# Performance work log

Hardware: AMD Instinct MI355X
Metric: run time of the kernel (lower is better)

The kernel has to match this reference:

```python
import jax, jax.numpy as jnp
import numpy as np

H, KVH, D, BS, L = 32, 8, 128, 16, 4096
MAX_BLOCKS = L // BS          # 256 blocks per sequence (sink cache capacity)
B = 16
NUM_BLOCKS = B * MAX_BLOCKS   # 4096 total cache blocks
T = MAX_BLOCKS * BS           # 4096 linearized cache slots per sequence
SCALE = 1.0 / np.sqrt(D)


def _rope_cos_sin(pos):
    # neox-style RoPE tables; pos: int array [...]. returns cos/sin [..., D/2]
    inv_freq = 1.0 / (10000.0 ** (jnp.arange(0, D, 2, dtype=jnp.float32) / D))
    ang = pos[..., None].astype(jnp.float32) * inv_freq
    return jnp.cos(ang), jnp.sin(ang)


def _apply_rope(x, cos, sin):
    # x [..., D]; cos/sin broadcastable to x[..., :D//2]
    x1, x2 = jnp.split(x, 2, axis=-1)
    return jnp.concatenate([x1 * cos - x2 * sin, x2 * cos + x1 * sin], axis=-1)


def setup_inputs() -> dict:
    key = jax.random.key(0)
    ks = jax.random.split(key, 6)
    q = jax.random.normal(ks[0], (B, H * D), dtype=jnp.float32)
    k = jax.random.normal(ks[1], (B, KVH * D), dtype=jnp.float32)
    v = jax.random.normal(ks[2], (B, KVH * D), dtype=jnp.float32)
    key_cache = jax.random.normal(ks[3], (NUM_BLOCKS, BS, KVH, D), dtype=jnp.float32)
    value_cache = jax.random.normal(ks[4], (NUM_BLOCKS, BS, KVH, D), dtype=jnp.float32)
    block_tables = jnp.arange(B * MAX_BLOCKS, dtype=jnp.int32).reshape(B, MAX_BLOCKS)
    context_lens = jax.random.randint(ks[5], (B,), 0, 6000, dtype=jnp.int32)
    return {"q": q, "k": k, "v": v, "key_cache": key_cache,
            "value_cache": value_cache, "block_tables": block_tables,
            "context_lens": context_lens}


def reference(q, k, v, key_cache, value_cache, block_tables, context_lens):
    ctx = context_lens.astype(jnp.int32)                         # [B] past tokens
    rem = ctx % BS
    # sink/rolling cap: if past >= model_context_len, effective seq len caps
    seq_len = jnp.where(ctx >= L, L - BS + rem + 1, ctx + 1)     # [B]
    pos_q = seq_len - 1                                          # capped current position

    # gather pre-rope keys/values from paged cache -> [B, T, KVH, D]
    keys = key_cache[block_tables].reshape(B, T, KVH, D)
    vals = value_cache[block_tables].reshape(B, T, KVH, D)

    # re-apply rope to gathered keys at their cache-relative positions 0..T-1
    cos_k, sin_k = _rope_cos_sin(jnp.arange(T))                  # [T, D/2]
    keys = _apply_rope(keys, cos_k[None, :, None, :], sin_k[None, :, None, :])

    # rope current q, k at capped positions
    cos_q, sin_q = _rope_cos_sin(pos_q)                          # [B, D/2]
    qh = _apply_rope(q.reshape(B, H, D), cos_q[:, None, :], sin_q[:, None, :])
    kh = _apply_rope(k.reshape(B, KVH, D), cos_q[:, None, :], sin_q[:, None, :])

    # scatter current token's k/v at its slot (offset rem in last used block == seq_len-1)
    bidx = jnp.arange(B)
    keys = keys.at[bidx, pos_q].set(kh)
    vals = vals.at[bidx, pos_q].set(v.reshape(B, KVH, D))

    # GQA attention over first seq_len cached tokens
    G = H // KVH
    qg = qh.reshape(B, KVH, G, D)
    scores = jnp.einsum('bhgd,bthd->bhgt', qg, keys) * SCALE     # [B, KVH, G, T]
    mask = jnp.arange(T)[None, :] < seq_len[:, None]             # [B, T]
    scores = jnp.where(mask[:, None, None, :], scores, jnp.finfo(scores.dtype).min)
    probs = jax.nn.softmax(scores, axis=-1)
    out = jnp.einsum('bhgt,bthd->bhgd', probs, vals)             # [B, KVH, G, D]
    return out.reshape(B, H * D)
```

## Files before the change

### kernel.cpp

```cpp
#include <hip/hip_runtime.h>
#include <math.h>

#define B_      16
#define H_      32
#define KVH_    8
#define G_      4
#define D_      128
#define BS_     16
#define L_      4096
#define MAXB_   256
#define T_      4096
#define NPART_  64
#define PART_   64
#define SCALE_  0.08838834764831843f

typedef unsigned long long ull;

__device__ __forceinline__ int seq_len_of(int ctx) {
  return (ctx >= L_) ? (L_ - BS_ + (ctx & (BS_ - 1)) + 1) : (ctx + 1);
}

__global__ void rope_table_kernel(float* __restrict__ tab) {
  int idx = blockIdx.x * blockDim.x + threadIdx.x;
  if (idx >= T_ * 64) return;
  int t = idx >> 6, i = idx & 63;
  double inv = pow(10000.0, -(double)(2 * i) / 128.0);
  float ang = (float)t * (float)inv;
  double a = (double)ang;
  tab[2 * idx]     = (float)cos(a);
  tab[2 * idx + 1] = (float)sin(a);
}


#define LOADK(P, tt)                                                        \
  {                                                                         \
    int tcl_  = min((tt), t1m1);                                            \
    int blk_  = (int)((packed >> (((tcl_ - t0) >> 4) * 16)) & 0xFFFF);      \
    int base_ = ((blk_ * BS_ + (tcl_ & (BS_ - 1))) * KVH_ + kvh) * D_;      \
    const float4* kc4_ = (const float4*)(kc + base_);                       \
    const float4* vc4_ = (const float4*)(vc + base_);                       \
    P##ka = kc4_[dg];      P##kb = kc4_[16 + dg];                           \
    P##va = vc4_[dg];      P##vb = vc4_[16 + dg];                           \
  }

#define COMPUTE(P, tt)                                                      \
  {                                                                         \
    float kr1[4], kr2[4];                                                   \
    kr1[0] = P##ka.x * cc0.x - P##kb.x * cc0.y;                             \
    kr2[0] = P##kb.x * cc0.x + P##ka.x * cc0.y;                             \
    kr1[1] = P##ka.y * cc0.z - P##kb.y * cc0.w;                             \
    kr2[1] = P##kb.y * cc0.z + P##ka.y * cc0.w;                             \
    kr1[2] = P##ka.z * cc1.x - P##kb.z * cc1.y;                             \
    kr2[2] = P##kb.z * cc1.x + P##ka.z * cc1.y;                             \
    kr1[3] = P##ka.w * cc1.z - P##kb.w * cc1.w;                             \
    kr2[3] = P##kb.w * cc1.z + P##ka.w * cc1.w;                             \
    bool valid_ = ((tt) < t1) & ((tt) != posq);                             \
    float s[G_];                                                            \
    _Pragma("unroll")                                                       \
    for (int g = 0; g < G_; ++g) {                                          \
      s[g] = kr1[0] * q1[g][0] + kr2[0] * q2[g][0]                          \
           + kr1[1] * q1[g][1] + kr2[1] * q2[g][1]                          \
           + kr1[2] * q1[g][2] + kr2[2] * q2[g][2]                          \
           + kr1[3] * q1[g][3] + kr2[3] * q2[g][3];                         \
    }                                                                       \
    _Pragma("unroll")                                                       \
    for (int off = 1; off <= 8; off <<= 1) {                                \
      _Pragma("unroll")                                                     \
      for (int g = 0; g < G_; ++g) s[g] += __shfl_xor(s[g], off);           \
    }                                                                       \
    _Pragma("unroll")                                                       \
    for (int g = 0; g < G_; ++g) {                                          \
      float sv   = valid_ ? s[g] : -1e30f;                                  \
      float mn   = fmaxf(m[g], sv);                                         \
      float corr = __expf(m[g] - mn);                                       \
      float p    = __expf(sv - mn);                                         \
      p = valid_ ? p : 0.0f;                                                \
      m[g] = mn;                                                            \
      l[g] = l[g] * corr + p;                                               \
      acc[g][0] = acc[g][0] * corr + p * P##va.x;                           \
      acc[g][1] = acc[g][1] * corr + p * P##va.y;                           \
      acc[g][2] = acc[g][2] * corr + p * P##va.z;                           \
      acc[g][3] = acc[g][3] * corr + p * P##va.w;                           \
      acc[g][4] = acc[g][4] * corr + p * P##vb.x;                           \
      acc[g][5] = acc[g][5] * corr + p * P##vb.y;                           \
      acc[g][6] = acc[g][6] * corr + p * P##vb.z;                           \
      acc[g][7] = acc[g][7] * corr + p * P##vb.w;                           \
    }                                                                       \
    {                      \
      float nc_;                                                            \
      nc_ = cc0.x * r0.x - cc0.y * r0.y;                                    \
      cc0.y = cc0.y * r0.x + cc0.x * r0.y; cc0.x = nc_;                     \
      nc_ = cc0.z * r0.z - cc0.w * r0.w;                                    \
      cc0.w = cc0.w * r0.z + cc0.z * r0.w; cc0.z = nc_;                     \
      nc_ = cc1.x * r1.x - cc1.y * r1.y;                                    \
      cc1.y = cc1.y * r1.x + cc1.x * r1.y; cc1.x = nc_;                     \
      nc_ = cc1.z * r1.z - cc1.w * r1.w;                                    \
      cc1.w = cc1.w * r1.z + cc1.z * r1.w; cc1.z = nc_;                     \
    }                                                                       \
  }

__global__ __launch_bounds__(256, 3) void attn_partial_kernel(
    const float* __restrict__ q, const float* __restrict__ knew,
    const float* __restrict__ vnew, const float* __restrict__ kc,
    const float* __restrict__ vc, const int* __restrict__ btab,
    const int* __restrict__ ctxl, const float* __restrict__ tab,
    float* __restrict__ opart, float2* __restrict__ ml) {
  int bid  = blockIdx.x;
  int wv   = threadIdx.x >> 6;
  int kvh  = (bid >> 4) & (KVH_ - 1);
  int b    = bid >> 7;
  int part = ((bid & 15) << 2) | wv;

  int seq = seq_len_of(ctxl[b]);
  int t0 = part * PART_;
  if (t0 >= seq) return;
  int t1 = min(t0 + PART_, seq);
  int t1m1 = t1 - 1;
  int posq = seq - 1;
  int pidx = ((b * KVH_ + kvh) * NPART_ + part) * G_;

  int lane = threadIdx.x & 63;
  int tsub = lane >> 4;
  int dg   = lane & 15;

  int4 bi = *(const int4*)(btab + b * MAXB_ + (t0 >> 4));
  ull packed = (ull)(unsigned)bi.x | ((ull)(unsigned)bi.y << 16)
             | ((ull)(unsigned)bi.z << 32) | ((ull)(unsigned)bi.w << 48);

  const float4* tab4 = (const float4*)tab;

  int tstart = t0 + tsub;
  float4 cc0 = tab4[tstart * 32 + 2 * dg];
  float4 cc1 = tab4[tstart * 32 + 2 * dg + 1];
  float4 r0  = tab4[4 * 32 + 2 * dg];
  float4 r1  = tab4[4 * 32 + 2 * dg + 1];

  float q1[G_][4], q2[G_][4];
  {
    float4 cq0 = tab4[posq * 32 + 2 * dg];
    float4 cq1 = tab4[posq * 32 + 2 * dg + 1];
#pragma unroll
    for (int g = 0; g < G_; ++g) {
      const float* qp = q + b * (H_ * D_) + (kvh * G_ + g) * D_;
      float4 a  = *(const float4*)(qp + 4 * dg);
      float4 bq = *(const float4*)(qp + 64 + 4 * dg);
      q1[g][0] = (a.x * cq0.x - bq.x * cq0.y) * SCALE_;
      q2[g][0] = (bq.x * cq0.x + a.x * cq0.y) * SCALE_;
      q1[g][1] = (a.y * cq0.z - bq.y * cq0.w) * SCALE_;
      q2[g][1] = (bq.y * cq0.z + a.y * cq0.w) * SCALE_;
      q1[g][2] = (a.z * cq1.x - bq.z * cq1.y) * SCALE_;
      q2[g][2] = (bq.z * cq1.x + a.z * cq1.y) * SCALE_;
      q1[g][3] = (a.w * cq1.z - bq.w * cq1.w) * SCALE_;
      q2[g][3] = (bq.w * cq1.z + a.w * cq1.w) * SCALE_;
    }
  }

  float m[G_], l[G_], acc[G_][8];
#pragma unroll
  for (int g = 0; g < G_; ++g) {
    m[g] = -1e30f; l[g] = 0.f;
#pragma unroll
    for (int j = 0; j < 8; ++j) acc[g][j] = 0.f;
  }

  {
    float4 Aka, Akb, Ava, Avb;
    float4 Bka, Bkb, Bva, Bvb;
    int nIter = (t1 - t0 + 3) >> 2;
    nIter = (nIter + 1) & ~1;
    int t = tstart;
    LOADK(A, t);
    for (int it = 0; it < nIter; it += 2) {
      LOADK(B, t + 4);  COMPUTE(A, t);  t += 4;
      LOADK(A, t + 4);  COMPUTE(B, t);  t += 4;
    }
  }

  if (lane < 16 && posq >= t0 && posq < t1) {
    const float* kp = knew + (b * KVH_ + kvh) * D_;
    float4 xa = *(const float4*)(kp + 4 * dg);
    float4 xb = *(const float4*)(kp + 64 + 4 * dg);
    float4 p0 = tab4[posq * 32 + 2 * dg];
    float4 p1 = tab4[posq * 32 + 2 * dg + 1];
    float kr1[4], kr2[4];
    kr1[0] = xa.x * p0.x - xb.x * p0.y;  kr2[0] = xb.x * p0.x + xa.x * p0.y;
    kr1[1] = xa.y * p0.z - xb.y * p0.w;  kr2[1] = xb.y * p0.z + xa.y * p0.w;
    kr1[2] = xa.z * p1.x - xb.z * p1.y;  kr2[2] = xb.z * p1.x + xa.z * p1.y;
    kr1[3] = xa.w * p1.z - xb.w * p1.w;  kr2[3] = xb.w * p1.z + xa.w * p1.w;
    const float* vp = vnew + (b * KVH_ + kvh) * D_;
    float4 va_ = *(const float4*)(vp + 4 * dg);
    float4 vb_ = *(const float4*)(vp + 64 + 4 * dg);
    float s[G_];
#pragma unroll
    for (int g = 0; g < G_; ++g) {
      s[g] = kr1[0] * q1[g][0] + kr2[0] * q2[g][0]
           + kr1[1] * q1[g][1] + kr2[1] * q2[g][1]
           + kr1[2] * q1[g][2] + kr2[2] * q2[g][2]
           + kr1[3] * q1[g][3] + kr2[3] * q2[g][3];
    }
#pragma unroll
    for (int off = 1; off <= 8; off <<= 1) {
#pragma unroll
      for (int g = 0; g < G_; ++g) s[g] += __shfl_xor(s[g], off);
    }
#pragma unroll
    for (int g = 0; g < G_; ++g) {
      float sv   = s[g];
      float mn   = fmaxf(m[g], sv);
      float corr = __expf(m[g] - mn);
      float p    = __expf(sv - mn);
      m[g] = mn;
      l[g] = l[g] * corr + p;
      acc[g][0] = acc[g][0] * corr + p * va_.x;
      acc[g][1] = acc[g][1] * corr + p * va_.y;
      acc[g][2] = acc[g][2] * corr + p * va_.z;
      acc[g][3] = acc[g][3] * corr + p * va_.w;
      acc[g][4] = acc[g][4] * corr + p * vb_.x;
      acc[g][5] = acc[g][5] * corr + p * vb_.y;
      acc[g][6] = acc[g][6] * corr + p * vb_.z;
      acc[g][7] = acc[g][7] * corr + p * vb_.w;
    }
  }

#pragma unroll
  for (int off = 16; off <= 32; off <<= 1) {
#pragma unroll
    for (int g = 0; g < G_; ++g) {
      float mo = __shfl_xor(m[g], off);
      float lo = __shfl_xor(l[g], off);
      float M  = fmaxf(m[g], mo);
      float fa = __expf(m[g] - M);
      float fb = __expf(mo - M);
      l[g] = l[g] * fa + lo * fb;
      m[g] = M;
#pragma unroll
      for (int j = 0; j < 8; ++j) {
        float ao = __shfl_xor(acc[g][j], off);
        acc[g][j] = acc[g][j] * fa + ao * fb;
      }
    }
  }

  if (lane < 16) {
#pragma unroll
    for (int g = 0; g < G_; ++g) {
      float* op = opart + (size_t)(pidx + g) * D_;
      *(float4*)(op + 4 * dg)      = make_float4(acc[g][0], acc[g][1], acc[g][2], acc[g][3]);
      *(float4*)(op + 64 + 4 * dg) = make_float4(acc[g][4], acc[g][5], acc[g][6], acc[g][7]);
      if (lane == 0) ml[pidx + g] = make_float2(m[g], l[g]);
    }
  }
}

__global__ void attn_reduce_kernel(const float* __restrict__ opart,
                                   const float2* __restrict__ ml,
                                   const int* __restrict__ ctxl,
                                   float* __restrict__ out) {
  int bh = blockIdx.x;
  int b = bh >> 5, h = bh & 31;
  int kvh = h >> 2, g = h & 3;
  int d = threadIdx.x;
  int seq = seq_len_of(ctxl[b]);
  int nlive = (seq + PART_ - 1) / PART_;
  int base = (b * KVH_ + kvh) * NPART_;

  float M = -1e30f;
  for (int p = 0; p < nlive; ++p) M = fmaxf(M, ml[(base + p) * G_ + g].x);
  float L = 0.f, O = 0.f;
  for (int p = 0; p < nlive; ++p) {
    float2 mlv = ml[(base + p) * G_ + g];
    float f = __expf(mlv.x - M);
    L += mlv.y * f;
    O += opart[(size_t)((base + p) * G_ + g) * D_ + d] * f;
  }
  out[b * (H_ * D_) + h * D_ + d] = O / L;
}

extern "C" void kernel_launch(void* const* d_in, const int* in_sizes, int n_in,
                              void* d_out, int out_size, void* d_ws, size_t ws_size,
                              hipStream_t stream) {
  const float* q    = (const float*)d_in[0];
  const float* k    = (const float*)d_in[1];
  const float* v    = (const float*)d_in[2];
  const float* kc   = (const float*)d_in[3];
  const float* vc   = (const float*)d_in[4];
  const int*   btab = (const int*)d_in[5];
  const int*   ctxl = (const int*)d_in[6];
  float* out = (float*)d_out;

  float*  tab   = (float*)d_ws;
  float*  opart = tab + (size_t)T_ * 64 * 2;
  float2* ml    = (float2*)(opart + (size_t)B_ * KVH_ * NPART_ * G_ * D_);

  rope_table_kernel<<<(T_ * 64 + 255) / 256, 256, 0, stream>>>(tab);
  attn_partial_kernel<<<B_ * KVH_ * (NPART_ / 4), 256, 0, stream>>>(
      q, k, v, kc, vc, btab, ctxl, tab, opart, ml);
  attn_reduce_kernel<<<B_ * H_, D_, 0, stream>>>(opart, ml, ctxl, out);
}
```

Before: 137.8 us.

## Stage contiguous KV token rows through double-buffered LDS across all heads

Each block now handles one 32-token partition for all 8 KV heads with 512 threads. It cooperatively loads full contiguous token rows (all heads) of K and V into double-buffered shared memory, then each wave computes its head from LDS. The aim is fully coalesced global reads in place of per-head strided 512-byte segments, with prefetch of the next group overlapping compute. The cost is a __syncthreads per 4-token group, LDS traffic, and twice as many partitions for the reduce kernel to combine.

```diff
diff --git a/kernel.cpp b/kernel.cpp
--- a/kernel.cpp
+++ b/kernel.cpp
@@ -10,11 +10,11 @@
 #define L_      4096
 #define MAXB_   256
 #define T_      4096
-#define NPART_  64
-#define PART_   64
+#define PARTN_  32
+#define NP_     (T_ / PARTN_)
+#define GT_     4
+#define TPAD_   1032
 #define SCALE_  0.08838834764831843f
-
-typedef unsigned long long ull;
 
 __device__ __forceinline__ int seq_len_of(int ctx) {
   return (ctx >= L_) ? (L_ - BS_ + (ctx & (BS_ - 1)) + 1) : (ctx + 1);
@@ -31,101 +31,33 @@
   tab[2 * idx + 1] = (float)sin(a);
 }
 
-
-#define LOADK(P, tt)                                                        \
-  {                                                                         \
-    int tcl_  = min((tt), t1m1);                                            \
-    int blk_  = (int)((packed >> (((tcl_ - t0) >> 4) * 16)) & 0xFFFF);      \
-    int base_ = ((blk_ * BS_ + (tcl_ & (BS_ - 1))) * KVH_ + kvh) * D_;      \
-    const float4* kc4_ = (const float4*)(kc + base_);                       \
-    const float4* vc4_ = (const float4*)(vc + base_);                       \
-    P##ka = kc4_[dg];      P##kb = kc4_[16 + dg];                           \
-    P##va = vc4_[dg];      P##vb = vc4_[16 + dg];                           \
-  }
-
-#define COMPUTE(P, tt)                                                      \
-  {                                                                         \
-    float kr1[4], kr2[4];                                                   \
-    kr1[0] = P##ka.x * cc0.x - P##kb.x * cc0.y;                             \
-    kr2[0] = P##kb.x * cc0.x + P##ka.x * cc0.y;                             \
-    kr1[1] = P##ka.y * cc0.z - P##kb.y * cc0.w;                             \
-    kr2[1] = P##kb.y * cc0.z + P##ka.y * cc0.w;                             \
-    kr1[2] = P##ka.z * cc1.x - P##kb.z * cc1.y;                             \
-    kr2[2] = P##kb.z * cc1.x + P##ka.z * cc1.y;                             \
-    kr1[3] = P##ka.w * cc1.z - P##kb.w * cc1.w;                             \
-    kr2[3] = P##kb.w * cc1.z + P##ka.w * cc1.w;                             \
-    bool valid_ = ((tt) < t1) & ((tt) != posq);                             \
-    float s[G_];                                                            \
-    _Pragma("unroll")                                                       \
-    for (int g = 0; g < G_; ++g) {                                          \
-      s[g] = kr1[0] * q1[g][0] + kr2[0] * q2[g][0]                          \
-           + kr1[1] * q1[g][1] + kr2[1] * q2[g][1]                          \
-           + kr1[2] * q1[g][2] + kr2[2] * q2[g][2]                          \
-           + kr1[3] * q1[g][3] + kr2[3] * q2[g][3];                         \
-    }                                                                       \
-    _Pragma("unroll")                                                       \
-    for (int off = 1; off <= 8; off <<= 1) {                                \
-      _Pragma("unroll")                                                     \
-      for (int g = 0; g < G_; ++g) s[g] += __shfl_xor(s[g], off);           \
-    }                                                                       \
-    _Pragma("unroll")                                                       \
-    for (int g = 0; g < G_; ++g) {                                          \
-      float sv   = valid_ ? s[g] : -1e30f;                                  \
-      float mn   = fmaxf(m[g], sv);                                         \
-      float corr = __expf(m[g] - mn);                                       \
-      float p    = __expf(sv - mn);                                         \
-      p = valid_ ? p : 0.0f;                                                \
-      m[g] = mn;                                                            \
-      l[g] = l[g] * corr + p;                                               \
-      acc[g][0] = acc[g][0] * corr + p * P##va.x;                           \
-      acc[g][1] = acc[g][1] * corr + p * P##va.y;                           \
-      acc[g][2] = acc[g][2] * corr + p * P##va.z;                           \
-      acc[g][3] = acc[g][3] * corr + p * P##va.w;                           \
-      acc[g][4] = acc[g][4] * corr + p * P##vb.x;                           \
-      acc[g][5] = acc[g][5] * corr + p * P##vb.y;                           \
-      acc[g][6] = acc[g][6] * corr + p * P##vb.z;                           \
-      acc[g][7] = acc[g][7] * corr + p * P##vb.w;                           \
-    }                                                                       \
-    {                      \
-      float nc_;                                                            \
-      nc_ = cc0.x * r0.x - cc0.y * r0.y;                                    \
-      cc0.y = cc0.y * r0.x + cc0.x * r0.y; cc0.x = nc_;                     \
-      nc_ = cc0.z * r0.z - cc0.w * r0.w;                                    \
-      cc0.w = cc0.w * r0.z + cc0.z * r0.w; cc0.z = nc_;                     \
-      nc_ = cc1.x * r1.x - cc1.y * r1.y;                                    \
-      cc1.y = cc1.y * r1.x + cc1.x * r1.y; cc1.x = nc_;                     \
-      nc_ = cc1.z * r1.z - cc1.w * r1.w;                                    \
-      cc1.w = cc1.w * r1.z + cc1.z * r1.w; cc1.z = nc_;                     \
-    }                                                                       \
-  }
-
-__global__ __launch_bounds__(256, 3) void attn_partial_kernel(
+__global__ __launch_bounds__(512, 4) void attn_partial_kernel(
     const float* __restrict__ q, const float* __restrict__ knew,
     const float* __restrict__ vnew, const float* __restrict__ kc,
     const float* __restrict__ vc, const int* __restrict__ btab,
     const int* __restrict__ ctxl, const float* __restrict__ tab,
     float* __restrict__ opart, float2* __restrict__ ml) {
   int bid  = blockIdx.x;
-  int wv   = threadIdx.x >> 6;
-  int kvh  = (bid >> 4) & (KVH_ - 1);
+  int part = bid & (NP_ - 1);
   int b    = bid >> 7;
-  int part = ((bid & 15) << 2) | wv;
 
   int seq = seq_len_of(ctxl[b]);
-  int t0 = part * PART_;
+  int t0 = part * PARTN_;
   if (t0 >= seq) return;
-  int t1 = min(t0 + PART_, seq);
-  int t1m1 = t1 - 1;
+  int t1 = min(t0 + PARTN_, seq);
   int posq = seq - 1;
-  int pidx = ((b * KVH_ + kvh) * NPART_ + part) * G_;
-
-  int lane = threadIdx.x & 63;
+  int nG = (t1 - t0 + GT_ - 1) >> 2;
+
+  int tid  = threadIdx.x;
+  int kvh  = tid >> 6;
+  int lane = tid & 63;
   int tsub = lane >> 4;
   int dg   = lane & 15;
-
-  int4 bi = *(const int4*)(btab + b * MAXB_ + (t0 >> 4));
-  ull packed = (ull)(unsigned)bi.x | ((ull)(unsigned)bi.y << 16)
-             | ((ull)(unsigned)bi.z << 32) | ((ull)(unsigned)bi.w << 48);
+  int pidx = ((b * KVH_ + kvh) * NP_ + part) * G_;
+
+  int2 bt = *(const int2*)(btab + b * MAXB_ + (t0 >> 4));
+
+  __shared__ float lds[2][2][GT_ * TPAD_];
 
   const float4* tab4 = (const float4*)tab;
 
@@ -163,17 +95,92 @@
     for (int j = 0; j < 8; ++j) acc[g][j] = 0.f;
   }
 
-  {
-    float4 Aka, Akb, Ava, Avb;
-    float4 Bka, Bkb, Bva, Bvb;
-    int nIter = (t1 - t0 + 3) >> 2;
-    nIter = (nIter + 1) & ~1;
-    int t = tstart;
-    LOADK(A, t);
-    for (int it = 0; it < nIter; it += 2) {
-      LOADK(B, t + 4);  COMPUTE(A, t);  t += 4;
-      LOADK(A, t + 4);  COMPUTE(B, t);  t += 4;
-    }
+  float4 s0, s1, s2, s3;
+  auto stage_load = [&](int gi) {
+    int tg   = t0 + gi * GT_;
+    int blk  = (gi & 4) ? bt.y : bt.x;
+    int slot = tg & (BS_ - 1);
+    size_t base = (size_t)(blk * BS_ + slot) * (KVH_ * D_);
+    const float4* kg = (const float4*)(kc + base);
+    const float4* vg = (const float4*)(vc + base);
+    s0 = kg[tid];  s1 = kg[tid + 512];
+    s2 = vg[tid];  s3 = vg[tid + 512];
+  };
+  auto stage_write = [&](int buf) {
+    int a0 = ((tid)       >> 8) * TPAD_ + (((tid)       & 255) << 2);
+    int a1 = ((tid + 512) >> 8) * TPAD_ + (((tid + 512) & 255) << 2);
+    *(float4*)&lds[buf][0][a0] = s0;
+    *(float4*)&lds[buf][0][a1] = s1;
+    *(float4*)&lds[buf][1][a0] = s2;
+    *(float4*)&lds[buf][1][a1] = s3;
+  };
+
+  auto compute = [&](int buf, int tg) {
+    int aK = tsub * TPAD_ + kvh * D_ + 4 * dg;
+    float4 ka = *(const float4*)&lds[buf][0][aK];
+    float4 kb = *(const float4*)&lds[buf][0][aK + 64];
+    float4 va = *(const float4*)&lds[buf][1][aK];
+    float4 vb = *(const float4*)&lds[buf][1][aK + 64];
+    int tt = tg + tsub;
+    float kr1[4], kr2[4];
+    kr1[0] = ka.x * cc0.x - kb.x * cc0.y;  kr2[0] = kb.x * cc0.x + ka.x * cc0.y;
+    kr1[1] = ka.y * cc0.z - kb.y * cc0.w;  kr2[1] = kb.y * cc0.z + ka.y * cc0.w;
+    kr1[2] = ka.z * cc1.x - kb.z * cc1.y;  kr2[2] = kb.z * cc1.x + ka.z * cc1.y;
+    kr1[3] = ka.w * cc1.z - kb.w * cc1.w;  kr2[3] = kb.w * cc1.z + ka.w * cc1.w;
+    bool valid = (tt < t1) & (tt != posq);
+    float s[G_];
+#pragma unroll
+    for (int g = 0; g < G_; ++g) {
+      s[g] = kr1[0] * q1[g][0] + kr2[0] * q2[g][0]
+           + kr1[1] * q1[g][1] + kr2[1] * q2[g][1]
+           + kr1[2] * q1[g][2] + kr2[2] * q2[g][2]
+           + kr1[3] * q1[g][3] + kr2[3] * q2[g][3];
+    }
+#pragma unroll
+    for (int off = 1; off <= 8; off <<= 1) {
+#pragma unroll
+      for (int g = 0; g < G_; ++g) s[g] += __shfl_xor(s[g], off);
+    }
+#pragma unroll
+    for (int g = 0; g < G_; ++g) {
+      float sv   = valid ? s[g] : -1e30f;
+      float mn   = fmaxf(m[g], sv);
+      float corr = __expf(m[g] - mn);
+      float p    = __expf(sv - mn);
+      p = valid ? p : 0.0f;
+      m[g] = mn;
+      l[g] = l[g] * corr + p;
+      acc[g][0] = acc[g][0] * corr + p * va.x;
+      acc[g][1] = acc[g][1] * corr + p * va.y;
+      acc[g][2] = acc[g][2] * corr + p * va.z;
+      acc[g][3] = acc[g][3] * corr + p * va.w;
+      acc[g][4] = acc[g][4] * corr + p * vb.x;
+      acc[g][5] = acc[g][5] * corr + p * vb.y;
+      acc[g][6] = acc[g][6] * corr + p * vb.z;
+      acc[g][7] = acc[g][7] * corr + p * vb.w;
+    }
+    float nc;
+    nc = cc0.x * r0.x - cc0.y * r0.y;
+    cc0.y = cc0.y * r0.x + cc0.x * r0.y; cc0.x = nc;
+    nc = cc0.z * r0.z - cc0.w * r0.w;
+    cc0.w = cc0.w * r0.z + cc0.z * r0.w; cc0.z = nc;
+    nc = cc1.x * r1.x - cc1.y * r1.y;
+    cc1.y = cc1.y * r1.x + cc1.x * r1.y; cc1.x = nc;
+    nc = cc1.z * r1.z - cc1.w * r1.w;
+    cc1.w = cc1.w * r1.z + cc1.z * r1.w; cc1.z = nc;
+  };
+
+  stage_load(0);
+  stage_write(0);
+  __syncthreads();
+  int cur = 0;
+  int nGm1 = nG - 1;
+  for (int gi = 0; gi < nG; ++gi) {
+    stage_load(min(gi + 1, nGm1));
+    compute(cur, t0 + gi * GT_);
+    stage_write(cur ^ 1);
+    __syncthreads();
+    cur ^= 1;
   }
 
   if (lane < 16 && posq >= t0 && posq < t1) {
@@ -188,8 +195,8 @@
     kr1[2] = xa.z * p1.x - xb.z * p1.y;  kr2[2] = xb.z * p1.x + xa.z * p1.y;
     kr1[3] = xa.w * p1.z - xb.w * p1.w;  kr2[3] = xb.w * p1.z + xa.w * p1.w;
     const float* vp = vnew + (b * KVH_ + kvh) * D_;
-    float4 va_ = *(const float4*)(vp + 4 * dg);
-    float4 vb_ = *(const float4*)(vp + 64 + 4 * dg);
+    float4 va = *(const float4*)(vp + 4 * dg);
+    float4 vb = *(const float4*)(vp + 64 + 4 * dg);
     float s[G_];
 #pragma unroll
     for (int g = 0; g < G_; ++g) {
@@ -211,14 +218,14 @@
       float p    = __expf(sv - mn);
       m[g] = mn;
       l[g] = l[g] * corr + p;
-      acc[g][0] = acc[g][0] * corr + p * va_.x;
-      acc[g][1] = acc[g][1] * corr + p * va_.y;
-      acc[g][2] = acc[g][2] * corr + p * va_.z;
-      acc[g][3] = acc[g][3] * corr + p * va_.w;
-      acc[g][4] = acc[g][4] * corr + p * vb_.x;
-      acc[g][5] = acc[g][5] * corr + p * vb_.y;
-      acc[g][6] = acc[g][6] * corr + p * vb_.z;
-      acc[g][7] = acc[g][7] * corr + p * vb_.w;
+      acc[g][0] = acc[g][0] * corr + p * va.x;
+      acc[g][1] = acc[g][1] * corr + p * va.y;
+      acc[g][2] = acc[g][2] * corr + p * va.z;
+      acc[g][3] = acc[g][3] * corr + p * va.w;
+      acc[g][4] = acc[g][4] * corr + p * vb.x;
+      acc[g][5] = acc[g][5] * corr + p * vb.y;
+      acc[g][6] = acc[g][6] * corr + p * vb.z;
+      acc[g][7] = acc[g][7] * corr + p * vb.w;
     }
   }
 
@@ -261,8 +268,8 @@
   int kvh = h >> 2, g = h & 3;
   int d = threadIdx.x;
   int seq = seq_len_of(ctxl[b]);
-  int nlive = (seq + PART_ - 1) / PART_;
-  int base = (b * KVH_ + kvh) * NPART_;
+  int nlive = (seq + PARTN_ - 1) / PARTN_;
+  int base = (b * KVH_ + kvh) * NP_;
 
   float M = -1e30f;
   for (int p = 0; p < nlive; ++p) M = fmaxf(M, ml[(base + p) * G_ + g].x);
@@ -290,10 +297,10 @@
 
   float*  tab   = (float*)d_ws;
   float*  opart = tab + (size_t)T_ * 64 * 2;
-  float2* ml    = (float2*)(opart + (size_t)B_ * KVH_ * NPART_ * G_ * D_);
+  float2* ml    = (float2*)(opart + (size_t)B_ * KVH_ * NP_ * G_ * D_);
 
   rope_table_kernel<<<(T_ * 64 + 255) / 256, 256, 0, stream>>>(tab);
-  attn_partial_kernel<<<B_ * KVH_ * (NPART_ / 4), 256, 0, stream>>>(
+  attn_partial_kernel<<<B_ * NP_, 512, 0, stream>>>(
       q, k, v, kc, vc, btab, ctxl, tab, opart, ml);
   attn_reduce_kernel<<<B_ * H_, D_, 0, stream>>>(opart, ml, ctxl, out);
 }
```

New measurement: 315.8 us. +129.2%, slower.
